# Kernel tuning notes

Hardware: AMD Instinct MI355X
Metric: run time of the kernel (lower is better)

The kernel has to match this reference:

```python
import jax, jax.numpy as jnp
import numpy as np

N_NODES = 50000
N_EDGES = 800000
EMBED_DIM = 128


def setup_inputs() -> dict:
    key = jax.random.key(0)
    ks = jax.random.split(key, 6)
    std = 1.0 / np.sqrt(EMBED_DIM)
    emb = jax.random.normal(ks[0], (N_NODES, EMBED_DIM), dtype=jnp.float32)
    edges = jax.random.randint(ks[1], (2, N_EDGES), 0, N_NODES, dtype=jnp.int64)
    # torch Linear weights: [out, in]; w initialized uniform(-std, std), bias 0
    w_weight = jax.random.uniform(ks[2], (EMBED_DIM, EMBED_DIM), dtype=jnp.float32, minval=-std, maxval=std)
    w_bias = jnp.zeros((EMBED_DIM,), dtype=jnp.float32)
    a_weight = jax.random.normal(ks[3], (2 * EMBED_DIM,), dtype=jnp.float32) * 0.05
    a_bias = jnp.zeros((1,), dtype=jnp.float32)
    trans_weight = jax.random.normal(ks[4], (EMBED_DIM, 2 * EMBED_DIM), dtype=jnp.float32) * 0.05
    trans_bias = jnp.zeros((EMBED_DIM,), dtype=jnp.float32)
    ln_gamma = jnp.ones((EMBED_DIM,), dtype=jnp.float32)
    ln_beta = jnp.zeros((EMBED_DIM,), dtype=jnp.float32)
    return {
        'emb': emb, 'edges': edges,
        'w_weight': w_weight, 'w_bias': w_bias,
        'a_weight': a_weight, 'a_bias': a_bias,
        'trans_weight': trans_weight, 'trans_bias': trans_bias,
        'ln_gamma': ln_gamma, 'ln_beta': ln_beta,
    }


def reference(emb, edges, w_weight, w_bias, a_weight, a_bias, trans_weight, trans_bias, ln_gamma, ln_beta):
    bsz, d = emb.shape
    e_dst, e_src = edges[0], edges[1]  # torch indexing: emb[edges[0]], emb[edges[1]]
    # w(emb) once per node: [N, d]
    s = emb @ w_weight.T + w_bias
    # a(concat(w(e0), w(e1))) = s[e0] @ a1 + s[e1] @ a2 + b -> per-node scalars, then gather
    a1, a2 = a_weight[:d], a_weight[d:]
    p1 = s @ a1  # [N]
    p2 = s @ a2  # [N]
    score = p1[e_dst] + p2[e_src] + a_bias[0]  # [E]
    # exp(leaky_relu(score, 0.2))
    attn = jnp.exp(jnp.where(score > 0, score, 0.2 * score))  # [E]
    # sparse row-sum of attention (spmm with ones vector)
    denom = jax.ops.segment_sum(attn, e_dst, num_segments=bsz)  # [N]
    # spmm: aggregate attn-weighted source embeddings per destination row
    msg = attn[:, None] * emb[e_src]  # [E, d]
    agg = jax.ops.segment_sum(msg, e_dst, num_segments=bsz)  # [N, d]
    agg = agg / (denom[:, None] + 1e-20)
    # trans(concat(emb, agg)) then LayerNorm
    h = jnp.concatenate([emb, agg], axis=-1) @ trans_weight.T + trans_bias
    mu = jnp.mean(h, axis=-1, keepdims=True)
    var = jnp.mean(jnp.square(h - mu), axis=-1, keepdims=True)
    h = (h - mu) * jax.lax.rsqrt(var + 1e-5) * ln_gamma + ln_beta
    return h
```

## Files before the change

kernel.cpp:

```cpp
#include <hip/hip_runtime.h>
#include <hip/hip_bf16.h>

#define NN 50000
#define NE 800000
#define DIM 128
#define NBKT 196
#define BKTCAP 4608
#define CAP 64
#define EPB 4096
#define NEB 196

typedef __attribute__((ext_vector_type(8))) short short8_t;
typedef __attribute__((ext_vector_type(8))) unsigned short ushort8_t;
typedef __attribute__((ext_vector_type(4))) float floatx4;

static __device__ inline unsigned short f2bf(float x){
  unsigned int u = __float_as_uint(x);
  unsigned int r = (u + 0x7FFF + ((u >> 16) & 1)) >> 16;
  return (unsigned short)r;
}
static __device__ inline float bf2f(unsigned short u){
  return __uint_as_float(((unsigned int)u) << 16);
}

__global__ __launch_bounds__(256) void k_setup(const float* __restrict__ W,
                       const float* __restrict__ wb,
                       const float* __restrict__ aw, const float* __restrict__ ab,
                       float* __restrict__ v12c,
                       const float4* __restrict__ T4, ushort4* __restrict__ Tb4,
                       int* __restrict__ gcount){
  int b = blockIdx.x;
  int t = threadIdx.x;
  if (b == 0){
    __shared__ float r1[DIM], r2[DIM];
    if (t < DIM){
      float s1 = 0.f, s2 = 0.f;
      for (int j = 0; j < DIM; ++j){
        float w = W[j*DIM + t];
        s1 += aw[j] * w;
        s2 += aw[DIM + j] * w;
      }
      v12c[t] = s1;
      v12c[DIM + t] = s2;
      float bb = wb[t];
      r1[t] = bb * aw[t];
      r2[t] = bb * aw[DIM + t];
    }
    __syncthreads();
    if (t == 0){
      float a1s = 0.f, a2s = 0.f;
      for (int j = 0; j < DIM; ++j){ a1s += r1[j]; a2s += r2[j]; }
      v12c[2*DIM]   = a1s + ab[0];
      v12c[2*DIM+1] = a2s;
    }
  } else if (b <= 32){
    int i = (b-1)*256 + t;
    float4 v = T4[i];
    Tb4[i] = make_ushort4(f2bf(v.x), f2bf(v.y), f2bf(v.z), f2bf(v.w));
  } else {
    int i = (b-33)*256 + t;
    if (i < NBKT*16) gcount[i] = 0;
  }
}

__global__ __launch_bounds__(256) void k_A(const float4* __restrict__ emb4,
                      const float* __restrict__ v12c,
                      float* __restrict__ p1, float* __restrict__ p2,
                      unsigned short* __restrict__ embh,
                      const int* __restrict__ dst, const int* __restrict__ srcp,
                      int* __restrict__ gcount, int* __restrict__ bpool){
  if (blockIdx.x < NEB){
    __shared__ int bcnt[NBKT], bbase[NBKT];
    int t = threadIdx.x;
    if (t < NBKT) bcnt[t] = 0;
    __syncthreads();
    int rnk[16], bkt[16], pk[16];
    #pragma unroll
    for (int j = 0; j < 16; ++j){
      int e = blockIdx.x * EPB + j*256 + t;
      bkt[j] = -1;
      if (e < NE){
        int d = dst[e], s = srcp[e];
        bkt[j] = d >> 8;
        pk[j] = ((d & 255) << 16) | s;
        rnk[j] = atomicAdd(&bcnt[bkt[j]], 1);
      }
    }
    __syncthreads();
    if (t < NBKT) bbase[t] = atomicAdd(&gcount[t*16], bcnt[t]);
    __syncthreads();
    #pragma unroll
    for (int j = 0; j < 16; ++j){
      if (bkt[j] >= 0){
        int pos = bbase[bkt[j]] + rnk[j];
        if (pos < BKTCAP) bpool[bkt[j]*BKTCAP + pos] = pk[j];
      }
    }
    return;
  }
  int g = threadIdx.x & 31;
  int i = (blockIdx.x - NEB) * 8 + (threadIdx.x >> 5);
  if (i >= NN) return;
  float4 e = emb4[i*32 + g];
  *(ushort4*)(embh + i*DIM + g*4) =
      make_ushort4(f2bf(e.x), f2bf(e.y), f2bf(e.z), f2bf(e.w));
  float4 a = ((const float4*)v12c)[g];
  float4 b = ((const float4*)v12c)[32 + g];
  float s1 = e.x*a.x + e.y*a.y + e.z*a.z + e.w*a.w;
  float s2 = e.x*b.x + e.y*b.y + e.z*b.z + e.w*b.w;
  #pragma unroll
  for (int off = 16; off; off >>= 1){
    s1 += __shfl_down(s1, off, 32);
    s2 += __shfl_down(s2, off, 32);
  }
  if (g == 0){
    p1[i] = s1 + v12c[256];
    p2[i] = s2 + v12c[257];
  }
}

__global__ __launch_bounds__(1024) void k_B(const int* __restrict__ gcount,
                      const int* __restrict__ bpool,
                      int* __restrict__ count, int* __restrict__ csr){
  __shared__ int cnt[256];
  int b = blockIdx.x, t = threadIdx.x;
  if (t < 256) cnt[t] = 0;
  __syncthreads();
  int m = gcount[b*16]; if (m > BKTCAP) m = BKTCAP;
  int base = b * BKTCAP;
  int rnk[5], pkv[5];
  #pragma unroll
  for (int it = 0; it < 5; ++it){
    int e = it*1024 + t;
    pkv[it] = -1;
    if (e < m){
      int pk = bpool[base + e];
      pkv[it] = pk;
      rnk[it] = atomicAdd(&cnt[(pk >> 16) & 255], 1);
    }
  }
  __syncthreads();
  if (t < 256){
    int n = b*256 + t;
    if (n < NN){ int c = cnt[t]; count[n] = c < CAP ? c : CAP; }
  }
  #pragma unroll
  for (int it = 0; it < 5; ++it){
    if (pkv[it] >= 0 && rnk[it] < CAP){
      int d = b*256 + ((pkv[it] >> 16) & 255);
      csr[(d << 6) + rnk[it]] = pkv[it] & 0xFFFF;
    }
  }
}

__global__ __launch_bounds__(256) void k_gather(const int* __restrict__ count,
                       const int* __restrict__ csr,
                       const float* __restrict__ p1, const float* __restrict__ p2,
                       const unsigned short* __restrict__ embh,
                       unsigned short* __restrict__ aggh){
  int lane = threadIdx.x & 63;
  int c16 = lane & 15;
  int g4 = lane >> 4;
  int n = blockIdx.x * 4 + (threadIdx.x >> 6);
  if (n >= NN) return;
  int cnt = count[n];
  int s0 = n << 6;
  float p1n = p1[n];
  float acc[8] = {0.f,0.f,0.f,0.f,0.f,0.f,0.f,0.f};
  float dsum = 0.f;
  for (int e = g4; e < cnt; e += 16){
    int e1 = e + 4, e2 = e + 8, e3 = e + 12;
    int sa = csr[s0 + e];
    int sb = csr[e1 < cnt ? s0 + e1 : s0];
    int sc = csr[e2 < cnt ? s0 + e2 : s0];
    int sd = csr[e3 < cnt ? s0 + e3 : s0];
    float fa = p1n + p2[sa];
    float fb = p1n + p2[sb];
    float fc = p1n + p2[sc];
    float fd = p1n + p2[sd];
    fa = fa > 0.f ? fa : 0.2f * fa;
    fb = fb > 0.f ? fb : 0.2f * fb;
    fc = fc > 0.f ? fc : 0.2f * fc;
    fd = fd > 0.f ? fd : 0.2f * fd;
    float aa = __expf(fa);
    float ab_ = (e1 < cnt) ? __expf(fb) : 0.f;
    float ac = (e2 < cnt) ? __expf(fc) : 0.f;
    float ad = (e3 < cnt) ? __expf(fd) : 0.f;
    dsum += aa + ab_ + ac + ad;
    const ushort8_t va = *(const ushort8_t*)(embh + sa*DIM + c16*8);
    const ushort8_t vb = *(const ushort8_t*)(embh + sb*DIM + c16*8);
    const ushort8_t vc = *(const ushort8_t*)(embh + sc*DIM + c16*8);
    const ushort8_t vd = *(const ushort8_t*)(embh + sd*DIM + c16*8);
    #pragma unroll
    for (int j = 0; j < 8; ++j){
      acc[j] += aa * bf2f(va[j]) + ab_ * bf2f(vb[j])
              + ac * bf2f(vc[j]) + ad * bf2f(vd[j]);
    }
  }
  #pragma unroll
  for (int j = 0; j < 8; ++j){
    acc[j] += __shfl_xor(acc[j], 16, 64);
    acc[j] += __shfl_xor(acc[j], 32, 64);
  }
  dsum += __shfl_xor(dsum, 16, 64);
  dsum += __shfl_xor(dsum, 32, 64);
  if (g4 == 0){
    float dinv = 1.0f / (dsum + 1e-20f);
    ushort8_t o;
    #pragma unroll
    for (int j = 0; j < 8; ++j) o[j] = f2bf(acc[j] * dinv);
    *(ushort8_t*)(aggh + n*DIM + c16*8) = o;
  }
}

__global__ __launch_bounds__(256) void k_out(const unsigned short* __restrict__ embh,
                     const unsigned short* __restrict__ aggh,
                     const unsigned short* __restrict__ Tb,
                     const float* __restrict__ tb,
                     const float* __restrict__ gamma, const float* __restrict__ beta,
                     float* __restrict__ out){
  int t = threadIdx.x;
  int w = t >> 6;
  int lane = t & 63;
  int m16 = lane & 15;
  int q = lane >> 4;
  int nodebase = blockIdx.x * 128 + w * 32;
  int nA0 = nodebase + m16;
  int nA1 = nodebase + 16 + m16;
  int nA0c = (nA0 < NN) ? nA0 : 0;
  int nA1c = (nA1 < NN) ? nA1 : 0;
  floatx4 acc[2][8];
  #pragma unroll
  for (int st = 0; st < 2; ++st)
    #pragma unroll
    for (int ct = 0; ct < 8; ++ct) acc[st][ct] = (floatx4){0.f, 0.f, 0.f, 0.f};

  #pragma unroll
  for (int kc = 0; kc < 8; ++kc){
    int k0 = kc*32 + q*8;
    const unsigned short* ap0 = (kc < 4) ? (embh + nA0c*DIM + k0)
                                         : (aggh + nA0c*DIM + (k0 - 128));
    const unsigned short* ap1 = (kc < 4) ? (embh + nA1c*DIM + k0)
                                         : (aggh + nA1c*DIM + (k0 - 128));
    short8_t afrag0 = *(const short8_t*)ap0;
    short8_t afrag1 = *(const short8_t*)ap1;
    #pragma unroll
    for (int ct = 0; ct < 8; ++ct){
      short8_t bfrag = *(const short8_t*)(Tb + (ct*16 + m16)*256 + k0);
      acc[0][ct] = __builtin_amdgcn_mfma_f32_16x16x32_bf16(afrag0, bfrag, acc[0][ct], 0, 0, 0);
      acc[1][ct] = __builtin_amdgcn_mfma_f32_16x16x32_bf16(afrag1, bfrag, acc[1][ct], 0, 0, 0);
    }
  }

  float tbv[8], gmv[8], btv[8];
  #pragma unroll
  for (int ct = 0; ct < 8; ++ct){
    int col = ct*16 + m16;
    tbv[ct] = tb[col]; gmv[ct] = gamma[col]; btv[ct] = beta[col];
  }
  #pragma unroll
  for (int st = 0; st < 2; ++st){
    #pragma unroll
    for (int r = 0; r < 4; ++r){
      int n = nodebase + st*16 + q*4 + r;
      float h[8]; float s = 0.f, ss = 0.f;
      #pragma unroll
      for (int ct = 0; ct < 8; ++ct){
        h[ct] = acc[st][ct][r] + tbv[ct];
        s += h[ct]; ss += h[ct]*h[ct];
      }
      #pragma unroll
      for (int off = 1; off < 16; off <<= 1){
        s  += __shfl_xor(s,  off, 16);
        ss += __shfl_xor(ss, off, 16);
      }
      float mu = s * (1.f/128.f);
      float var = ss * (1.f/128.f) - mu*mu;
      float rstd = rsqrtf(var + 1e-5f);
      if (n < NN){
        #pragma unroll
        for (int ct = 0; ct < 8; ++ct){
          out[n*DIM + ct*16 + m16] = (h[ct]-mu)*rstd*gmv[ct] + btv[ct];
        }
      }
    }
  }
}

extern "C" void kernel_launch(void* const* d_in, const int* in_sizes, int n_in,
                              void* d_out, int out_size, void* d_ws, size_t ws_size,
                              hipStream_t stream){
  const float* emb          = (const float*)d_in[0];
  const int*   edges        = (const int*)d_in[1];
  const float* w_weight     = (const float*)d_in[2];
  const float* w_bias       = (const float*)d_in[3];
  const float* a_weight     = (const float*)d_in[4];
  const float* a_bias       = (const float*)d_in[5];
  const float* trans_weight = (const float*)d_in[6];
  const float* trans_bias   = (const float*)d_in[7];
  const float* ln_gamma     = (const float*)d_in[8];
  const float* ln_beta      = (const float*)d_in[9];
  float* out = (float*)d_out;

  float* ws      = (float*)d_ws;
  float* p1      = ws;
  float* p2      = ws + 50000;
  float* v12c    = ws + 100000;
  int*   count   = (int*)(ws + 100320);
  int*   gcount  = (int*)(ws + 150320);
  int*   csr     = (int*)(ws + 153472);
  int*   bpool   = (int*)(ws + 3353472);
  unsigned short* embh = (unsigned short*)(ws + 4256640);
  unsigned short* aggh = (unsigned short*)(ws + 7456640);
  unsigned short* Tb   = (unsigned short*)(ws + 10656640);

  const int* e_dst = edges;
  const int* e_src = edges + NE;

  k_setup<<<46, 256, 0, stream>>>(w_weight, w_bias, a_weight, a_bias, v12c,
                                  (const float4*)trans_weight, (ushort4*)Tb, gcount);
  k_A<<<NEB + (NN + 7)/8, 256, 0, stream>>>((const float4*)emb, v12c, p1, p2,
                                            embh, e_dst, e_src, gcount, bpool);
  k_B<<<NBKT, 1024, 0, stream>>>(gcount, bpool, count, csr);
  k_gather<<<(NN + 3)/4, 256, 0, stream>>>(count, csr, p1, p2, embh, aggh);
  k_out<<<(NN + 127)/128, 256, 0, stream>>>(embh, aggh, Tb, trans_bias,
                                            ln_gamma, ln_beta, out);
}
```

Baseline: 171.3 us.

## Fuse neighbor gather with output projection and LayerNorm via shared memory

Merges the gather/aggregation kernel and the output MFMA+LayerNorm kernel into one 1024-thread kernel handling 16 nodes per block. Aggregated rows stay in LDS instead of going to a global bf16 buffer, and each of 8 waves computes a 16-column slice of the projection, with LayerNorm statistics reduced across waves through shared memory. This removes a kernel launch and the global write and reread of the aggregate. In exchange, the MFMA work is split into smaller per-wave tiles and adds block-wide syncs, so the gather waves and the matmul waves can no longer overlap freely.

Result: slower. 212.0 us (+23.8%).

```diff
diff --git a/kernel.cpp b/kernel.cpp
--- a/kernel.cpp
+++ b/kernel.cpp
@@ -153,16 +153,23 @@
   }
 }
 
-__global__ __launch_bounds__(256) void k_gather(const int* __restrict__ count,
+__global__ __launch_bounds__(1024) void k_go(const int* __restrict__ count,
                        const int* __restrict__ csr,
                        const float* __restrict__ p1, const float* __restrict__ p2,
                        const unsigned short* __restrict__ embh,
-                       unsigned short* __restrict__ aggh){
-  int lane = threadIdx.x & 63;
+                       const unsigned short* __restrict__ Tb,
+                       const float* __restrict__ tb,
+                       const float* __restrict__ gamma, const float* __restrict__ beta,
+                       float* __restrict__ out){
+  __shared__ unsigned short sagg[16][DIM + 8];
+  __shared__ float ssum[8][16], ssq[8][16];
+  int t = threadIdx.x;
+  int w = t >> 6;
+  int lane = t & 63;
   int c16 = lane & 15;
   int g4 = lane >> 4;
-  int n = blockIdx.x * 4 + (threadIdx.x >> 6);
-  if (n >= NN) return;
+  int nodebase = blockIdx.x * 16;
+  int n = nodebase + w;
   int cnt = count[n];
   int s0 = n << 6;
   float p1n = p1[n];
@@ -209,80 +216,49 @@
     ushort8_t o;
     #pragma unroll
     for (int j = 0; j < 8; ++j) o[j] = f2bf(acc[j] * dinv);
-    *(ushort8_t*)(aggh + n*DIM + c16*8) = o;
-  }
-}
-
-__global__ __launch_bounds__(256) void k_out(const unsigned short* __restrict__ embh,
-                     const unsigned short* __restrict__ aggh,
-                     const unsigned short* __restrict__ Tb,
-                     const float* __restrict__ tb,
-                     const float* __restrict__ gamma, const float* __restrict__ beta,
-                     float* __restrict__ out){
-  int t = threadIdx.x;
-  int w = t >> 6;
-  int lane = t & 63;
-  int m16 = lane & 15;
-  int q = lane >> 4;
-  int nodebase = blockIdx.x * 128 + w * 32;
-  int nA0 = nodebase + m16;
-  int nA1 = nodebase + 16 + m16;
-  int nA0c = (nA0 < NN) ? nA0 : 0;
-  int nA1c = (nA1 < NN) ? nA1 : 0;
-  floatx4 acc[2][8];
-  #pragma unroll
-  for (int st = 0; st < 2; ++st)
-    #pragma unroll
-    for (int ct = 0; ct < 8; ++ct) acc[st][ct] = (floatx4){0.f, 0.f, 0.f, 0.f};
-
-  #pragma unroll
-  for (int kc = 0; kc < 8; ++kc){
-    int k0 = kc*32 + q*8;
-    const unsigned short* ap0 = (kc < 4) ? (embh + nA0c*DIM + k0)
-                                         : (aggh + nA0c*DIM + (k0 - 128));
-    const unsigned short* ap1 = (kc < 4) ? (embh + nA1c*DIM + k0)
-                                         : (aggh + nA1c*DIM + (k0 - 128));
-    short8_t afrag0 = *(const short8_t*)ap0;
-    short8_t afrag1 = *(const short8_t*)ap1;
-    #pragma unroll
-    for (int ct = 0; ct < 8; ++ct){
-      short8_t bfrag = *(const short8_t*)(Tb + (ct*16 + m16)*256 + k0);
-      acc[0][ct] = __builtin_amdgcn_mfma_f32_16x16x32_bf16(afrag0, bfrag, acc[0][ct], 0, 0, 0);
-      acc[1][ct] = __builtin_amdgcn_mfma_f32_16x16x32_bf16(afrag1, bfrag, acc[1][ct], 0, 0, 0);
-    }
-  }
-
-  float tbv[8], gmv[8], btv[8];
-  #pragma unroll
-  for (int ct = 0; ct < 8; ++ct){
-    int col = ct*16 + m16;
-    tbv[ct] = tb[col]; gmv[ct] = gamma[col]; btv[ct] = beta[col];
-  }
-  #pragma unroll
-  for (int st = 0; st < 2; ++st){
+    *(ushort8_t*)(&sagg[w][c16*8]) = o;
+  }
+  __syncthreads();
+  float hs[4];
+  if (w < 8){
+    int nAr = nodebase + c16;
+    floatx4 facc = (floatx4){0.f, 0.f, 0.f, 0.f};
+    #pragma unroll
+    for (int kc = 0; kc < 8; ++kc){
+      int k0 = kc*32 + g4*8;
+      short8_t afrag = (kc < 4)
+        ? *(const short8_t*)(embh + nAr*DIM + k0)
+        : *(const short8_t*)(&sagg[c16][k0 - 128]);
+      short8_t bfrag = *(const short8_t*)(Tb + (w*16 + c16)*256 + k0);
+      facc = __builtin_amdgcn_mfma_f32_16x16x32_bf16(afrag, bfrag, facc, 0, 0, 0);
+    }
+    float tbv = tb[w*16 + c16];
     #pragma unroll
     for (int r = 0; r < 4; ++r){
-      int n = nodebase + st*16 + q*4 + r;
-      float h[8]; float s = 0.f, ss = 0.f;
-      #pragma unroll
-      for (int ct = 0; ct < 8; ++ct){
-        h[ct] = acc[st][ct][r] + tbv[ct];
-        s += h[ct]; ss += h[ct]*h[ct];
-      }
+      float h = facc[r] + tbv;
+      hs[r] = h;
+      float sr = h, qr = h*h;
       #pragma unroll
       for (int off = 1; off < 16; off <<= 1){
-        s  += __shfl_xor(s,  off, 16);
-        ss += __shfl_xor(ss, off, 16);
+        sr += __shfl_xor(sr, off, 16);
+        qr += __shfl_xor(qr, off, 16);
       }
+      if (c16 == 0){ ssum[w][g4*4 + r] = sr; ssq[w][g4*4 + r] = qr; }
+    }
+  }
+  __syncthreads();
+  if (w < 8){
+    float gmv = gamma[w*16 + c16], btv = beta[w*16 + c16];
+    #pragma unroll
+    for (int r = 0; r < 4; ++r){
+      int row = g4*4 + r;
+      float s = 0.f, q2 = 0.f;
+      #pragma unroll
+      for (int ww = 0; ww < 8; ++ww){ s += ssum[ww][row]; q2 += ssq[ww][row]; }
       float mu = s * (1.f/128.f);
-      float var = ss * (1.f/128.f) - mu*mu;
+      float var = q2 * (1.f/128.f) - mu*mu;
       float rstd = rsqrtf(var + 1e-5f);
-      if (n < NN){
-        #pragma unroll
-        for (int ct = 0; ct < 8; ++ct){
-          out[n*DIM + ct*16 + m16] = (h[ct]-mu)*rstd*gmv[ct] + btv[ct];
-        }
-      }
+      out[(nodebase + row)*DIM + w*16 + c16] = (hs[r]-mu)*rstd*gmv + btv;
     }
   }
 }
@@ -311,7 +287,6 @@
   int*   csr     = (int*)(ws + 153472);
   int*   bpool   = (int*)(ws + 3353472);
   unsigned short* embh = (unsigned short*)(ws + 4256640);
-  unsigned short* aggh = (unsigned short*)(ws + 7456640);
   unsigned short* Tb   = (unsigned short*)(ws + 10656640);
 
   const int* e_dst = edges;
@@ -322,7 +297,6 @@
   k_A<<<NEB + (NN + 7)/8, 256, 0, stream>>>((const float4*)emb, v12c, p1, p2,
                                             embh, e_dst, e_src, gcount, bpool);
   k_B<<<NBKT, 1024, 0, stream>>>(gcount, bpool, count, csr);
-  k_gather<<<(NN + 3)/4, 256, 0, stream>>>(count, csr, p1, p2, embh, aggh);
-  k_out<<<(NN + 127)/128, 256, 0, stream>>>(embh, aggh, Tb, trans_bias,
-                                            ln_gamma, ln_beta, out);
-}
+  k_go<<<NN/16, 1024, 0, stream>>>(count, csr, p1, p2, embh, Tb, trans_bias,
+                                   ln_gamma, ln_beta, out);
+}
```
